# Kernel optimization log

Hardware: AMD Instinct MI355X
Metric: run time of the kernel (lower is better)

The kernel has to match this reference:

```python
import jax, jax.numpy as jnp
import numpy as np

B, S, N, DEG, KC = 4, 12, 8192, 16, 3
SEQ = S - KC + 1  # 10
H, LAYER, HID, MLP_H = 4, 3, 3, 64
NEG = -1e9


def setup_inputs() -> dict:
    key = jax.random.key(0)
    ks = jax.random.split(key, 40)
    f = lambda i, shp, sc=0.2: jax.random.normal(ks[i], shp, jnp.float32) * sc
    # deterministic unique edge list: DEG distinct neighbors per source node
    src = np.repeat(np.arange(N), DEG)
    dst = (src + 1 + np.tile(np.arange(DEG), N) * 37) % N
    edges = jnp.asarray(np.stack([src, dst]).astype(np.int32))
    return dict(
        occ=jax.random.normal(ks[0], (B, S, N), jnp.float32),
        prc_l=jax.random.uniform(ks[1], (B, N), jnp.float32),
        edges=edges,
        values=jnp.ones((N * DEG,), jnp.float32),
        conv_w=f(2, (1, 1, KC, 2)), conv_b=f(3, (1,)),
        gat_W=f(4, (H, SEQ, SEQ)), gat_a=f(5, (H, 2 * SEQ)),
        gat_lin_w=f(6, (1, H)), gat_lin_b=f(7, (1,)),
        gcn_w=f(8, (SEQ, SEQ)), gcn_b=f(9, (SEQ,)),
        Wih0=f(10, (4 * HID, LAYER)), Whh0=f(11, (4 * HID, HID)), bih0=f(12, (4 * HID,)), bhh0=f(13, (4 * HID,)),
        Wih1=f(14, (4 * HID, HID)), Whh1=f(15, (4 * HID, HID)), bih1=f(16, (4 * HID,)), bhh1=f(17, (4 * HID,)),
        Qw=f(18, (SEQ, SEQ)), Kw=f(19, (SEQ, SEQ)), Vw=f(20, (SEQ, SEQ)),
        m1w1=f(21, (MLP_H, SEQ)), m1b1=f(22, (MLP_H,)),
        m1w2=f(23, (MLP_H // 2, MLP_H)), m1b2=f(24, (MLP_H // 2,)),
        m1w3=f(25, (1, MLP_H // 2)), m1b3=f(26, (1,)),
        m2w1=f(27, (8 * (LAYER + 1), LAYER + 1)), m2b1=f(28, (8 * (LAYER + 1),)),
        m2w2=f(29, (4 * (LAYER + 1), 8 * (LAYER + 1))), m2b2=f(30, (4 * (LAYER + 1),)),
        m2w3=f(31, (1, 4 * (LAYER + 1))), m2b3=f(32, (1,)),
    )


def _lstm_layer(x, Wih, Whh, bih, bhh):
    # x: [T, Bn, in] time-major; PyTorch gate order i,f,g,o
    Bn, hdim = x.shape[1], Whh.shape[1]
    def step(carry, xt):
        h, c = carry
        g = xt @ Wih.T + h @ Whh.T + bih + bhh
        i, fg, gg, o = jnp.split(g, 4, axis=1)
        c = jax.nn.sigmoid(fg) * c + jax.nn.sigmoid(i) * jnp.tanh(gg)
        h = jax.nn.sigmoid(o) * jnp.tanh(c)
        return (h, c), h
    init = (jnp.zeros((Bn, hdim), x.dtype), jnp.zeros((Bn, hdim), x.dtype))
    _, hs = jax.lax.scan(step, init, x)
    return hs  # [T, Bn, hdim]


def _gat(x2, src, dst, values, mask, gat_W, gat_a, lin_w, lin_b):
    # x2: [b*n, seq]; only first N rows are gathered (faithful to the original)
    h = jnp.einsum('ns,hso->hno', x2, gat_W)                 # [H, b*n, seq]
    eh = jnp.concatenate([h[:, src, :], h[:, dst, :]], 2)    # [H, E, 2*seq]
    atts = jax.nn.leaky_relu(jnp.einsum('hed,hd->he', eh, gat_a), 0.2)  # [H, E]
    mt = atts.T @ lin_w.T + lin_b                            # [E, 1]
    new_vals = values * mt[:, 0]
    n = mask.shape[0]
    dense = jnp.zeros((n, n), x2.dtype).at[src, dst].add(new_vals)
    return jax.nn.softmax(dense + mask, axis=0)              # softmax over dim 0, as nn.Softmax(dim=0)


def reference(occ, prc_l, edges, values, conv_w, conv_b, gat_W, gat_a, gat_lin_w, gat_lin_b, gcn_w, gcn_b, Wih0, Whh0, bih0, bhh0, Wih1, Whh1, bih1, bhh1, Qw, Kw, Vw, m1w1, m1b1, m1w2, m1b2, m1w3, m1b3, m2w1, m2b1, m2w2, m2b2, m2w3, m2b3):
    b, s, n = occ.shape
    seq = s - conv_w.shape[2] + 1
    occ_t = jnp.transpose(occ, (0, 2, 1))                    # [b, n, s]
    prc = jnp.broadcast_to(prc_l[:, :, None], (b, n, s))
    fea = jnp.stack([occ_t, prc], axis=3).reshape(b * n, s, 2)[:, None]  # [bn,1,s,2]
    fea = jax.lax.conv_general_dilated(fea, conv_w, (1, 1), 'VALID',
                                       dimension_numbers=('NCHW', 'OIHW', 'NCHW'))
    fea = (fea + conv_b[None, :, None, None]).reshape(b, n, seq)
    src, dst = edges[0], edges[1]
    mask = jnp.full((n, n), NEG, occ.dtype).at[src, dst].set(0.0)
    lrelu = lambda z: jax.nn.leaky_relu(z, 0.01)
    gcn = lambda z: lrelu(z @ gcn_w.T + gcn_b)
    A1 = _gat(fea.reshape(b * n, seq), src, dst, values, mask, gat_W, gat_a, gat_lin_w, gat_lin_b)
    c1 = gcn(jnp.einsum('nm,bms->bns', A1, fea))
    A2 = _gat(c1.reshape(b * n, seq), src, dst, values, mask, gat_W, gat_a, gat_lin_w, gat_lin_b)
    c2 = gcn(jnp.einsum('nm,bms->bns', A2, c1))
    xt = jnp.stack([fea, c1, c2], axis=3).reshape(b * n, seq, 3)
    xT = jnp.transpose(xt, (1, 0, 2))                        # time-major [seq, bn, 3]
    h0 = _lstm_layer(xT, Wih0, Whh0, bih0, bhh0)
    h1 = _lstm_layer(h0, Wih1, Whh1, bih1, bhh1)
    x_long = jnp.transpose(h1, (1, 0, 2))                    # [bn, seq, 3]
    y_long = x_long[:, -1, 0]                                # [bn]
    xl = jnp.transpose(x_long, (0, 2, 1))                    # [bn, 3, seq]
    Q = xl @ Qw.T
    K = xl @ Kw.T
    V = xl @ Vw.T
    alpha = jax.nn.softmax(jnp.einsum('bis,bjs->bij', Q, K) / jnp.float32(V.shape[1]), axis=2)
    att = jnp.einsum('bij,bjs->bis', alpha, V)               # [bn, 3, seq]
    h = jax.nn.relu(att @ m1w1.T + m1b1)
    h = jax.nn.relu(h @ m1w2.T + m1b2)
    att_out = (h @ m1w3.T + m1b3)[:, :, 0]                   # [bn, 3]
    temp = jnp.concatenate([y_long[:, None], att_out], axis=1)  # [bn, 4]
    h = jax.nn.relu(temp @ m2w1.T + m2b1)
    h = jax.nn.relu(h @ m2w2.T + m2b2)
    y = (h @ m2w3.T + m2b3)[:, 0]
    return y.reshape(b, n)
```

## Files before the change

kernel.cpp:

```cpp
#include <hip/hip_runtime.h>

#define NN    8192
#define BB    4
#define SS    12
#define SEQL  10
#define SEQP  16
#define KCC   3
#define DEGN  16
#define EE    (NN*DEGN)
#define HHH   4
#define HIDN  3
#define BN    (BB*NN)

__device__ __forceinline__ float fexp(float x)  { return __expf(x); }
__device__ __forceinline__ float fsig(float x)  { return __fdividef(1.0f, 1.0f + __expf(-x)); }

__global__ __launch_bounds__(256) void k_fea_node(const float* __restrict__ occ,
                                                  const float* __restrict__ prc,
                                                  const float* __restrict__ convw,
                                                  const float* __restrict__ convb,
                                                  const float* __restrict__ gatW,
                                                  const float* __restrict__ gata,
                                                  float* __restrict__ fea,
                                                  float* __restrict__ p1p2) {
    int t = blockIdx.x * blockDim.x + threadIdx.x;
    if (t >= BN) return;
    int b = t >> 13, nn = t & (NN - 1);
    float o[SS];
    const float* op = occ + (size_t)b * SS * NN + nn;
#pragma unroll
    for (int s = 0; s < SS; s++) o[s] = op[(size_t)s * NN];
    float w0[KCC], w1s = 0.f;
#pragma unroll
    for (int k = 0; k < KCC; k++) { w0[k] = convw[k * 2]; w1s += convw[k * 2 + 1]; }
    float base = prc[t] * w1s + convb[0];
    float fv[SEQL];
#pragma unroll
    for (int tt = 0; tt < SEQL; tt++) {
        float acc = base;
#pragma unroll
        for (int k = 0; k < KCC; k++) acc += o[tt + k] * w0[k];
        fv[tt] = acc;
    }
    float* f = fea + (size_t)t * SEQP;
    *(float4*)(f)     = make_float4(fv[0], fv[1], fv[2], fv[3]);
    *(float4*)(f + 4) = make_float4(fv[4], fv[5], fv[6], fv[7]);
    *(float2*)(f + 8) = make_float2(fv[8], fv[9]);
    if (t < NN) {
#pragma unroll
        for (int hh = 0; hh < HHH; hh++) {
            float p1 = 0.f, p2 = 0.f;
#pragma unroll
            for (int oo = 0; oo < SEQL; oo++) {
                float hv = 0.f;
#pragma unroll
                for (int s = 0; s < SEQL; s++) hv += fv[s] * gatW[hh * (SEQL * SEQL) + s * SEQL + oo];
                p1 += hv * gata[hh * (2 * SEQL) + oo];
                p2 += hv * gata[hh * (2 * SEQL) + SEQL + oo];
            }
            p1p2[t * 8 + hh]     = p1;
            p1p2[t * 8 + 4 + hh] = p2;
        }
    }
}

__global__ __launch_bounds__(256) void k_colmt(const float* __restrict__ values,
                                               const float* __restrict__ p1p2,
                                               const float* __restrict__ linw,
                                               const float* __restrict__ linb,
                                               float* __restrict__ mt,
                                               float2* __restrict__ colms) {
    int u = blockIdx.x * blockDim.x + threadIdx.x;
    int q = u & 3, j = u >> 2;
    float p2l[HHH], lw[HHH];
#pragma unroll
    for (int hh = 0; hh < HHH; hh++) { p2l[hh] = p1p2[j * 8 + 4 + hh]; lw[hh] = linw[hh]; }
    float lb = linb[0];
    float v[4];
#pragma unroll
    for (int dd = 0; dd < 4; dd++) {
        int d = q * 4 + dd;
        int s = (j - 1 - d * 37) & (NN - 1);
        int e = s * DEGN + d;
        float4 p1v = *(const float4*)(p1p2 + s * 8);
        float a0 = p1v.x + p2l[0]; a0 = a0 > 0.f ? a0 : 0.2f * a0;
        float a1 = p1v.y + p2l[1]; a1 = a1 > 0.f ? a1 : 0.2f * a1;
        float a2 = p1v.z + p2l[2]; a2 = a2 > 0.f ? a2 : 0.2f * a2;
        float a3 = p1v.w + p2l[3]; a3 = a3 > 0.f ? a3 : 0.2f * a3;
        float acc = lb + a0*lw[0] + a1*lw[1] + a2*lw[2] + a3*lw[3];
        float m_ = acc * values[e];
        v[dd] = m_;
        mt[e] = m_;
    }
    float m = fmaxf(fmaxf(v[0], v[1]), fmaxf(v[2], v[3]));
    m = fmaxf(m, __shfl_xor(m, 1));
    m = fmaxf(m, __shfl_xor(m, 2));
    float sum = 0.f;
#pragma unroll
    for (int dd = 0; dd < 4; dd++) sum += fexp(v[dd] - m);
    sum += __shfl_xor(sum, 1);
    sum += __shfl_xor(sum, 2);
    if (q == 0) colms[j] = make_float2(m, __fdividef(1.0f, sum));
}

template <int DOP>
__global__ __launch_bounds__(256) void k_agg(const int* __restrict__ edges,
                                             const float* __restrict__ mt,
                                             const float2* __restrict__ colms,
                                             const float* __restrict__ xin,
                                             const float* __restrict__ gcnw,
                                             const float* __restrict__ gcnb,
                                             const float* __restrict__ gatW,
                                             const float* __restrict__ gata,
                                             float* __restrict__ xout,
                                             float* __restrict__ p1p2) {
    int u = blockIdx.x * blockDim.x + threadIdx.x;
    int q = u & 3, t = u >> 2;
    int b = t >> 13, i = t & (NN - 1);
    int e0 = i * DEGN + q * 4;
    int4   dn4 = *(const int4*)(edges + EE + e0);
    float4 mt4 = *(const float4*)(mt + e0);
    int dns[4] = {dn4.x, dn4.y, dn4.z, dn4.w};
    float mts[4] = {mt4.x, mt4.y, mt4.z, mt4.w};
    float acc[SEQL];
#pragma unroll
    for (int s = 0; s < SEQL; s++) acc[s] = 0.f;
#pragma unroll
    for (int dd = 0; dd < 4; dd++) {
        int dn = dns[dd];
        float2 ms = colms[dn];
        float w = fexp(mts[dd] - ms.x) * ms.y;
        const float* xr = xin + ((size_t)b * NN + dn) * SEQP;
        float4 v0 = *(const float4*)(xr);
        float4 v1 = *(const float4*)(xr + 4);
        float2 v2 = *(const float2*)(xr + 8);
        acc[0] += w*v0.x; acc[1] += w*v0.y; acc[2] += w*v0.z; acc[3] += w*v0.w;
        acc[4] += w*v1.x; acc[5] += w*v1.y; acc[6] += w*v1.z; acc[7] += w*v1.w;
        acc[8] += w*v2.x; acc[9] += w*v2.y;
    }
#pragma unroll
    for (int s = 0; s < SEQL; s++) acc[s] += __shfl_xor(acc[s], 1);
#pragma unroll
    for (int s = 0; s < SEQL; s++) acc[s] += __shfl_xor(acc[s], 2);

    float co[SEQL];
#pragma unroll
    for (int o = 0; o < SEQL; o++) {
        float a = gcnb[o];
#pragma unroll
        for (int s = 0; s < SEQL; s++) a += acc[s] * gcnw[o * SEQL + s];
        co[o] = a > 0.f ? a : 0.01f * a;
    }
    if (q == 0) {
        float* xo = xout + (size_t)t * SEQP;
        *(float4*)(xo)     = make_float4(co[0], co[1], co[2], co[3]);
        *(float4*)(xo + 4) = make_float4(co[4], co[5], co[6], co[7]);
        *(float2*)(xo + 8) = make_float2(co[8], co[9]);
    }
    if (DOP && t < NN) {
        float hv[SEQL];
#pragma unroll
        for (int oo = 0; oo < SEQL; oo++) hv[oo] = 0.f;
#pragma unroll
        for (int s = 0; s < SEQL; s++) {
            const float2* wr = (const float2*)(gatW + q * (SEQL*SEQL) + s * SEQL);
#pragma unroll
            for (int p = 0; p < 5; p++) {
                float2 wv = wr[p];
                hv[2*p]   += co[s] * wv.x;
                hv[2*p+1] += co[s] * wv.y;
            }
        }
        const float2* ga1 = (const float2*)(gata + q * (2*SEQL));
        const float2* ga2 = (const float2*)(gata + q * (2*SEQL) + SEQL);
        float p1 = 0.f, p2 = 0.f;
#pragma unroll
        for (int p = 0; p < 5; p++) {
            float2 a1 = ga1[p], a2 = ga2[p];
            p1 += hv[2*p] * a1.x + hv[2*p+1] * a1.y;
            p2 += hv[2*p] * a2.x + hv[2*p+1] * a2.y;
        }
        p1p2[t * 8 + q]     = p1;
        p1p2[t * 8 + 4 + q] = p2;
    }
}

__global__ __launch_bounds__(256) void k_lstm_att(
    const float* __restrict__ fea, const float* __restrict__ c1g, const float* __restrict__ c2g,
    const float* __restrict__ Wih0, const float* __restrict__ Whh0,
    const float* __restrict__ bih0, const float* __restrict__ bhh0,
    const float* __restrict__ Wih1, const float* __restrict__ Whh1,
    const float* __restrict__ bih1, const float* __restrict__ bhh1,
    const float* __restrict__ Qw, const float* __restrict__ Kw, const float* __restrict__ Vw,
    float* __restrict__ attrow) {

    int u = blockIdx.x * blockDim.x + threadIdx.x;
    int e = u & 1;
    int t = u >> 1;

    float fr[SEQL], c1r[SEQL], c2r[SEQL];
    {
        const float* a = fea + (size_t)t * SEQP;
        const float* b = c1g + (size_t)t * SEQP;
        const float* c = c2g + (size_t)t * SEQP;
        float4 a0 = *(const float4*)a, a1 = *(const float4*)(a+4); float2 a2 = *(const float2*)(a+8);
        float4 b0 = *(const float4*)b, b1 = *(const float4*)(b+4); float2 b2 = *(const float2*)(b+8);
        float4 d0 = *(const float4*)c, d1 = *(const float4*)(c+4); float2 d2 = *(const float2*)(c+8);
        fr[0]=a0.x; fr[1]=a0.y; fr[2]=a0.z; fr[3]=a0.w; fr[4]=a1.x; fr[5]=a1.y; fr[6]=a1.z; fr[7]=a1.w; fr[8]=a2.x; fr[9]=a2.y;
        c1r[0]=b0.x; c1r[1]=b0.y; c1r[2]=b0.z; c1r[3]=b0.w; c1r[4]=b1.x; c1r[5]=b1.y; c1r[6]=b1.z; c1r[7]=b1.w; c1r[8]=b2.x; c1r[9]=b2.y;
        c2r[0]=d0.x; c2r[1]=d0.y; c2r[2]=d0.z; c2r[3]=d0.w; c2r[4]=d1.x; c2r[5]=d1.y; c2r[6]=d1.z; c2r[7]=d1.w; c2r[8]=d2.x; c2r[9]=d2.y;
    }

    int r0 = e * 6;
    float W0[6][6], B0[6], W1[6][6], B1[6];
#pragma unroll
    for (int k = 0; k < 6; k++) {
        int r = r0 + k;
        W0[k][0]=Wih0[r*3]; W0[k][1]=Wih0[r*3+1]; W0[k][2]=Wih0[r*3+2];
        W0[k][3]=Whh0[r*3]; W0[k][4]=Whh0[r*3+1]; W0[k][5]=Whh0[r*3+2];
        B0[k]=bih0[r]+bhh0[r];
        W1[k][0]=Wih1[r*3]; W1[k][1]=Wih1[r*3+1]; W1[k][2]=Wih1[r*3+2];
        W1[k][3]=Whh1[r*3]; W1[k][4]=Whh1[r*3+1]; W1[k][5]=Whh1[r*3+2];
        B1[k]=bih1[r]+bhh1[r];
    }
    float two_e = e ? 2.f : 1.f;
    float neg_e = e ? -1.f : 0.f;

    float c0[3]={0,0,0}, c1s[3]={0,0,0}, h0[3]={0,0,0}, h1[3]={0,0,0};
    float hist[SEQL][HIDN];
#pragma unroll
    for (int st = 0; st < SEQL; st++) {
        float tt[6], pp[6];
        {
            float x0 = fr[st], x1 = c1r[st], x2 = c2r[st];
#pragma unroll
            for (int k = 0; k < 6; k++) {
                float g = B0[k] + x0*W0[k][0] + x1*W0[k][1] + x2*W0[k][2]
                                + h0[0]*W0[k][3] + h0[1]*W0[k][4] + h0[2]*W0[k][5];
                if (k < 3) { float uu = fsig(two_e * g); tt[k] = two_e * uu + neg_e; }
                else       { tt[k] = fsig(g); }
            }
#pragma unroll
            for (int k = 0; k < 6; k++) pp[k] = __shfl_xor(tt[k], 1);
#pragma unroll
            for (int j = 0; j < 3; j++) {
                float si = e ? pp[j]   : tt[j];
                float sf = e ? pp[3+j] : tt[3+j];
                float tg = e ? tt[j]   : pp[j];
                float so = e ? tt[3+j] : pp[3+j];
                float cn = sf * c0[j] + si * tg;
                c0[j] = cn;
                h0[j] = so * (2.f * fsig(2.f * cn) - 1.f);
            }
        }
        {
#pragma unroll
            for (int k = 0; k < 6; k++) {
                float g = B1[k] + h0[0]*W1[k][0] + h0[1]*W1[k][1] + h0[2]*W1[k][2]
                                + h1[0]*W1[k][3] + h1[1]*W1[k][4] + h1[2]*W1[k][5];
                if (k < 3) { float uu = fsig(two_e * g); tt[k] = two_e * uu + neg_e; }
                else       { tt[k] = fsig(g); }
            }
#pragma unroll
            for (int k = 0; k < 6; k++) pp[k] = __shfl_xor(tt[k], 1);
#pragma unroll
            for (int j = 0; j < 3; j++) {
                float si = e ? pp[j]   : tt[j];
                float sf = e ? pp[3+j] : tt[3+j];
                float tg = e ? tt[j]   : pp[j];
                float so = e ? tt[3+j] : pp[3+j];
                float cn = sf * c1s[j] + si * tg;
                c1s[j] = cn;
                h1[j] = so * (2.f * fsig(2.f * cn) - 1.f);
            }
        }
#pragma unroll
        for (int j = 0; j < 3; j++) hist[st][j] = h1[j];
    }

    float V[3][5];
    float sc[3][3];
#pragma unroll
    for (int a = 0; a < 3; a++)
#pragma unroll
        for (int j = 0; j < 3; j++) sc[a][j] = 0.f;
#pragma unroll
    for (int p = 0; p < 5; p++) {
        int o = 2 * p + e;
        float wq[SEQL], wk[SEQL], wv[SEQL];
        const float2* q2 = (const float2*)(Qw + o * SEQL);
        const float2* k2 = (const float2*)(Kw + o * SEQL);
        const float2* v2 = (const float2*)(Vw + o * SEQL);
#pragma unroll
        for (int z = 0; z < 5; z++) {
            float2 a = q2[z], b = k2[z], c = v2[z];
            wq[2*z] = a.x; wq[2*z+1] = a.y;
            wk[2*z] = b.x; wk[2*z+1] = b.y;
            wv[2*z] = c.x; wv[2*z+1] = c.y;
        }
        float qj[3], kj[3];
#pragma unroll
        for (int j = 0; j < 3; j++) {
            float qv = 0.f, kv = 0.f, vv = 0.f;
#pragma unroll
            for (int s = 0; s < SEQL; s++) {
                float xv = hist[s][j];
                qv += xv * wq[s]; kv += xv * wk[s]; vv += xv * wv[s];
            }
            qj[j] = qv; kj[j] = kv; V[j][p] = vv;
        }
#pragma unroll
        for (int a = 0; a < 3; a++)
#pragma unroll
            for (int j = 0; j < 3; j++) sc[a][j] += qj[a] * kj[j];
    }
#pragma unroll
    for (int a = 0; a < 3; a++)
#pragma unroll
        for (int j = 0; j < 3; j++) sc[a][j] += __shfl_xor(sc[a][j], 1);

    float* ar = attrow + (size_t)t * 32;
#pragma unroll
    for (int a = 0; a < 3; a++) {
        float s0 = sc[a][0] * (1.f/3.f), s1 = sc[a][1] * (1.f/3.f), s2 = sc[a][2] * (1.f/3.f);
        float m = fmaxf(s0, fmaxf(s1, s2));
        float e0 = fexp(s0-m), e1 = fexp(s1-m), e2 = fexp(s2-m);
        float inv = __fdividef(1.0f, e0 + e1 + e2);
#pragma unroll
        for (int p = 0; p < 5; p++)
            ar[a * SEQL + 2*p + e] = (e0*V[0][p] + e1*V[1][p] + e2*V[2][p]) * inv;
    }
    if (e == 0) ar[30] = hist[SEQL-1][0];
}

__global__ __launch_bounds__(256, 4) void k_head(
    const float* __restrict__ attrow,
    const float* __restrict__ m1w1, const float* __restrict__ m1b1,
    const float* __restrict__ m1w2, const float* __restrict__ m1b2,
    const float* __restrict__ m1w3, const float* __restrict__ m1b3,
    const float* __restrict__ m2w1, const float* __restrict__ m2b1,
    const float* __restrict__ m2w2, const float* __restrict__ m2b2,
    const float* __restrict__ m2w3, const float* __restrict__ m2b3,
    float* __restrict__ out) {

    __shared__ float lw[3717];
    int tid = threadIdx.x;
    for (int z = tid; z < 1024; z += 256) {
        int qq = z >> 8, kk = (z >> 4) & 15, s = z & 15;
        if (s < 12) lw[qq*200 + kk*12 + s] = (s < 10) ? m1w1[(qq*16+kk)*10 + s] : 0.f;
    }
    for (int z = tid; z < 2048; z += 256) {
        int qq = z >> 9, rem = z & 511, r = rem >> 4, kk = rem & 15;
        lw[800 + qq*520 + r*16 + kk] = m1w2[r*64 + qq*16 + kk];
    }
    for (int z = tid; z < 64;  z += 256) lw[2880 + z] = m1b1[z];
    for (int z = tid; z < 32;  z += 256) { lw[2944 + z] = m1b2[z]; lw[2976 + z] = m1w3[z]; }
    for (int z = tid; z < 128; z += 256) lw[3012 + z] = m2w1[z];
    for (int z = tid; z < 32;  z += 256) lw[3140 + z] = m2b1[z];
    for (int z = tid; z < 512; z += 256) lw[3172 + z] = m2w2[z];
    for (int z = tid; z < 16;  z += 256) { lw[3684 + z] = m2b2[z]; lw[3700 + z] = m2w3[z]; }
    if (tid == 0) { lw[3008] = m1b3[0]; lw[3716] = m2b3[0]; }
    __syncthreads();

    int u = blockIdx.x * blockDim.x + tid;
    int q = u & 3;
    int t = u >> 2;

    const float* w1b = lw + q * 200;
    float hb0[16], hb1[16], hb2a[16];
    float ylong;
    {
        float row[32];
        const float4* arp = (const float4*)(attrow + (size_t)t * 32);
#pragma unroll
        for (int p = 0; p < 8; p++) {
            float4 z = arp[p];
            row[4*p] = z.x; row[4*p+1] = z.y; row[4*p+2] = z.z; row[4*p+3] = z.w;
        }
        ylong = row[30];
#pragma unroll 4
        for (int kk = 0; kk < 16; kk++) {
            float4 wa = *(const float4*)(w1b + kk*12);
            float4 wb = *(const float4*)(w1b + kk*12 + 4);
            float4 wc = *(const float4*)(w1b + kk*12 + 8);
            float bk = lw[2880 + q*16 + kk];
            float a0 = bk
                + row[0]*wa.x + row[1]*wa.y + row[2]*wa.z + row[3]*wa.w
                + row[4]*wb.x + row[5]*wb.y + row[6]*wb.z + row[7]*wb.w
                + row[8]*wc.x + row[9]*wc.y;
            float a1 = bk
                + row[10]*wa.x + row[11]*wa.y + row[12]*wa.z + row[13]*wa.w
                + row[14]*wb.x + row[15]*wb.y + row[16]*wb.z + row[17]*wb.w
                + row[18]*wc.x + row[19]*wc.y;
            float a2 = bk
                + row[20]*wa.x + row[21]*wa.y + row[22]*wa.z + row[23]*wa.w
                + row[24]*wb.x + row[25]*wb.y + row[26]*wb.z + row[27]*wb.w
                + row[28]*wc.x + row[29]*wc.y;
            hb0[kk] = a0 > 0.f ? a0 : 0.f;
            hb1[kk] = a1 > 0.f ? a1 : 0.f;
            hb2a[kk] = a2 > 0.f ? a2 : 0.f;
        }
    }

    const float* w2b = lw + 800 + q * 520;
    float ao0 = lw[3008], ao1 = ao0, ao2 = ao0;
#pragma unroll 2
    for (int r = 0; r < 32; r++) {
        const float4* wr = (const float4*)(w2b + r * 16);
        float4 w0 = wr[0], w1 = wr[1], w2 = wr[2], w3 = wr[3];
        float p0 = hb0[0]*w0.x + hb0[1]*w0.y + hb0[2]*w0.z + hb0[3]*w0.w
                 + hb0[4]*w1.x + hb0[5]*w1.y + hb0[6]*w1.z + hb0[7]*w1.w
                 + hb0[8]*w2.x + hb0[9]*w2.y + hb0[10]*w2.z + hb0[11]*w2.w
                 + hb0[12]*w3.x + hb0[13]*w3.y + hb0[14]*w3.z + hb0[15]*w3.w;
        float p1 = hb1[0]*w0.x + hb1[1]*w0.y + hb1[2]*w0.z + hb1[3]*w0.w
                 + hb1[4]*w1.x + hb1[5]*w1.y + hb1[6]*w1.z + hb1[7]*w1.w
                 + hb1[8]*w2.x + hb1[9]*w2.y + hb1[10]*w2.z + hb1[11]*w2.w
                 + hb1[12]*w3.x + hb1[13]*w3.y + hb1[14]*w3.z + hb1[15]*w3.w;
        float p2 = hb2a[0]*w0.x + hb2a[1]*w0.y + hb2a[2]*w0.z + hb2a[3]*w0.w
                 + hb2a[4]*w1.x + hb2a[5]*w1.y + hb2a[6]*w1.z + hb2a[7]*w1.w
                 + hb2a[8]*w2.x + hb2a[9]*w2.y + hb2a[10]*w2.z + hb2a[11]*w2.w
                 + hb2a[12]*w3.x + hb2a[13]*w3.y + hb2a[14]*w3.z + hb2a[15]*w3.w;
        p0 += __shfl_xor(p0, 1); p0 += __shfl_xor(p0, 2);
        p1 += __shfl_xor(p1, 1); p1 += __shfl_xor(p1, 2);
        p2 += __shfl_xor(p2, 1); p2 += __shfl_xor(p2, 2);
        float bb = lw[2944 + r], ww = lw[2976 + r];
        float t0 = p0 + bb; t0 = t0 > 0.f ? t0 : 0.f;
        float t1 = p1 + bb; t1 = t1 > 0.f ? t1 : 0.f;
        float t2 = p2 + bb; t2 = t2 > 0.f ? t2 : 0.f;
        ao0 += t0 * ww; ao1 += t1 * ww; ao2 += t2 * ww;
    }

    float hb2[32];
#pragma unroll 8
    for (int k = 0; k < 32; k++) {
        float4 wv = *(const float4*)(lw + 3012 + k*4);
        float a = lw[3140 + k] + ylong*wv.x + ao0*wv.y + ao1*wv.z + ao2*wv.w;
        hb2[k] = a > 0.f ? a : 0.f;
    }
    float y = lw[3716];
#pragma unroll 4
    for (int r = 0; r < 16; r++) {
        float a = lw[3684 + r];
        const float4* wr = (const float4*)(lw + 3172 + r*32);
#pragma unroll
        for (int c = 0; c < 8; c++) {
            float4 wv = wr[c];
            a += hb2[4*c]*wv.x + hb2[4*c+1]*wv.y + hb2[4*c+2]*wv.z + hb2[4*c+3]*wv.w;
        }
        float h = a > 0.f ? a : 0.f;
        y += h * lw[3700 + r];
    }
    if (q == 0) out[t] = y;
}

extern "C" void kernel_launch(void* const* d_in, const int* in_sizes, int n_in,
                              void* d_out, int out_size, void* d_ws, size_t ws_size,
                              hipStream_t stream) {
    const float* occ    = (const float*)d_in[0];
    const float* prc    = (const float*)d_in[1];
    const int*   edges  = (const int*)  d_in[2];
    const float* values = (const float*)d_in[3];
    const float* convw  = (const float*)d_in[4];
    const float* convb  = (const float*)d_in[5];
    const float* gatW   = (const float*)d_in[6];
    const float* gata   = (const float*)d_in[7];
    const float* linw   = (const float*)d_in[8];
    const float* linb   = (const float*)d_in[9];
    const float* gcnw   = (const float*)d_in[10];
    const float* gcnb   = (const float*)d_in[11];
    const float* Wih0   = (const float*)d_in[12];
    const float* Whh0   = (const float*)d_in[13];
    const float* bih0   = (const float*)d_in[14];
    const float* bhh0   = (const float*)d_in[15];
    const float* Wih1   = (const float*)d_in[16];
    const float* Whh1   = (const float*)d_in[17];
    const float* bih1   = (const float*)d_in[18];
    const float* bhh1   = (const float*)d_in[19];
    const float* Qw     = (const float*)d_in[20];
    const float* Kw     = (const float*)d_in[21];
    const float* Vw     = (const float*)d_in[22];
    const float* m1w1   = (const float*)d_in[23];
    const float* m1b1   = (const float*)d_in[24];
    const float* m1w2   = (const float*)d_in[25];
    const float* m1b2   = (const float*)d_in[26];
    const float* m1w3   = (const float*)d_in[27];
    const float* m1b3   = (const float*)d_in[28];
    const float* m2w1   = (const float*)d_in[29];
    const float* m2b1   = (const float*)d_in[30];
    const float* m2w2   = (const float*)d_in[31];
    const float* m2b2   = (const float*)d_in[32];
    const float* m2w3   = (const float*)d_in[33];
    const float* m2b3   = (const float*)d_in[34];
    float* out = (float*)d_out;

    char* ws = (char*)d_ws;
    float*  fea    = (float*) (ws);
    float*  c1     = (float*) (ws + 2097152);
    float*  c2     = (float*) (ws + 4194304);
    float*  p1p2   = (float*) (ws + 6291456);
    float*  mt     = (float*) (ws + 6553600);
    float2* colms  = (float2*)(ws + 7077888);
    float*  attrow = (float*) (ws + 7143424);

    k_fea_node<<<128, 256, 0, stream>>>(occ, prc, convw, convb, gatW, gata, fea, p1p2);

    k_colmt<<<128, 256, 0, stream>>>(values, p1p2, linw, linb, mt, colms);
    k_agg<1><<<512, 256, 0, stream>>>(edges, mt, colms, fea, gcnw, gcnb,
                                      gatW, gata, c1, p1p2);

    k_colmt<<<128, 256, 0, stream>>>(values, p1p2, linw, linb, mt, colms);
    k_agg<0><<<512, 256, 0, stream>>>(edges, mt, colms, c1, gcnw, gcnb,
                                      gatW, gata, c2, p1p2);

    k_lstm_att<<<256, 256, 0, stream>>>(fea, c1, c2,
        Wih0, Whh0, bih0, bhh0, Wih1, Whh1, bih1, bhh1, Qw, Kw, Vw, attrow);

    k_head<<<512, 256, 0, stream>>>(attrow,
        m1w1, m1b1, m1w2, m1b2, m1w3, m1b3,
        m2w1, m2b1, m2w2, m2b2, m2w3, m2b3, out);
}
```

Before: 81.73 us.

## Split LSTM-attention per node across four lanes, one gate per lane

The fused LSTM plus attention kernel now gives each node four lanes instead of two. Each lane computes the three units of one gate type, and the gates are exchanged with xor-1 and xor-2 shuffles. The Q/K/V output columns are strided by four, with a guard for the last partial group. This doubles the thread count (512 blocks) and shortens the per-thread serial recurrence to get more latency hiding and parallelism, at the cost of more shuffles, redundant input loads and idle lanes in the attention stage.

```diff
diff --git a/kernel.cpp b/kernel.cpp
--- a/kernel.cpp
+++ b/kernel.cpp
@@ -195,8 +195,8 @@
     float* __restrict__ attrow) {
 
     int u = blockIdx.x * blockDim.x + threadIdx.x;
-    int e = u & 1;
-    int t = u >> 1;
+    int e = u & 3;
+    int t = u >> 2;
 
     float fr[SEQL], c1r[SEQL], c2r[SEQL];
     {
@@ -211,11 +211,10 @@
         c2r[0]=d0.x; c2r[1]=d0.y; c2r[2]=d0.z; c2r[3]=d0.w; c2r[4]=d1.x; c2r[5]=d1.y; c2r[6]=d1.z; c2r[7]=d1.w; c2r[8]=d2.x; c2r[9]=d2.y;
     }
 
-    int r0 = e * 6;
-    float W0[6][6], B0[6], W1[6][6], B1[6];
-#pragma unroll
-    for (int k = 0; k < 6; k++) {
-        int r = r0 + k;
+    float W0[3][6], B0[3], W1[3][6], B1[3];
+#pragma unroll
+    for (int k = 0; k < 3; k++) {
+        int r = e * 3 + k;
         W0[k][0]=Wih0[r*3]; W0[k][1]=Wih0[r*3+1]; W0[k][2]=Wih0[r*3+2];
         W0[k][3]=Whh0[r*3]; W0[k][4]=Whh0[r*3+1]; W0[k][5]=Whh0[r*3+2];
         B0[k]=bih0[r]+bhh0[r];
@@ -223,31 +222,33 @@
         W1[k][3]=Whh1[r*3]; W1[k][4]=Whh1[r*3+1]; W1[k][5]=Whh1[r*3+2];
         B1[k]=bih1[r]+bhh1[r];
     }
-    float two_e = e ? 2.f : 1.f;
-    float neg_e = e ? -1.f : 0.f;
+    float two_e = (e == 2) ? 2.f : 1.f;
+    float neg_e = (e == 2) ? -1.f : 0.f;
 
     float c0[3]={0,0,0}, c1s[3]={0,0,0}, h0[3]={0,0,0}, h1[3]={0,0,0};
     float hist[SEQL][HIDN];
 #pragma unroll
     for (int st = 0; st < SEQL; st++) {
-        float tt[6], pp[6];
+        float tt[3], pp[3], qq[3], rr[3];
         {
             float x0 = fr[st], x1 = c1r[st], x2 = c2r[st];
 #pragma unroll
-            for (int k = 0; k < 6; k++) {
+            for (int k = 0; k < 3; k++) {
                 float g = B0[k] + x0*W0[k][0] + x1*W0[k][1] + x2*W0[k][2]
                                 + h0[0]*W0[k][3] + h0[1]*W0[k][4] + h0[2]*W0[k][5];
-                if (k < 3) { float uu = fsig(two_e * g); tt[k] = two_e * uu + neg_e; }
-                else       { tt[k] = fsig(g); }
-            }
-#pragma unroll
-            for (int k = 0; k < 6; k++) pp[k] = __shfl_xor(tt[k], 1);
+                float uu = fsig(two_e * g);
+                tt[k] = two_e * uu + neg_e;
+            }
+#pragma unroll
+            for (int k = 0; k < 3; k++) pp[k] = __shfl_xor(tt[k], 1);
+#pragma unroll
+            for (int k = 0; k < 3; k++) { qq[k] = __shfl_xor(tt[k], 2); rr[k] = __shfl_xor(pp[k], 2); }
 #pragma unroll
             for (int j = 0; j < 3; j++) {
-                float si = e ? pp[j]   : tt[j];
-                float sf = e ? pp[3+j] : tt[3+j];
-                float tg = e ? tt[j]   : pp[j];
-                float so = e ? tt[3+j] : pp[3+j];
+                float si = (e==0)?tt[j]:(e==1)?pp[j]:(e==2)?qq[j]:rr[j];
+                float sf = (e==0)?pp[j]:(e==1)?tt[j]:(e==2)?rr[j]:qq[j];
+                float tg = (e==0)?qq[j]:(e==1)?rr[j]:(e==2)?tt[j]:pp[j];
+                float so = (e==0)?rr[j]:(e==1)?qq[j]:(e==2)?pp[j]:tt[j];
                 float cn = sf * c0[j] + si * tg;
                 c0[j] = cn;
                 h0[j] = so * (2.f * fsig(2.f * cn) - 1.f);
@@ -255,20 +256,22 @@
         }
         {
 #pragma unroll
-            for (int k = 0; k < 6; k++) {
+            for (int k = 0; k < 3; k++) {
                 float g = B1[k] + h0[0]*W1[k][0] + h0[1]*W1[k][1] + h0[2]*W1[k][2]
                                 + h1[0]*W1[k][3] + h1[1]*W1[k][4] + h1[2]*W1[k][5];
-                if (k < 3) { float uu = fsig(two_e * g); tt[k] = two_e * uu + neg_e; }
-                else       { tt[k] = fsig(g); }
-            }
-#pragma unroll
-            for (int k = 0; k < 6; k++) pp[k] = __shfl_xor(tt[k], 1);
+                float uu = fsig(two_e * g);
+                tt[k] = two_e * uu + neg_e;
+            }
+#pragma unroll
+            for (int k = 0; k < 3; k++) pp[k] = __shfl_xor(tt[k], 1);
+#pragma unroll
+            for (int k = 0; k < 3; k++) { qq[k] = __shfl_xor(tt[k], 2); rr[k] = __shfl_xor(pp[k], 2); }
 #pragma unroll
             for (int j = 0; j < 3; j++) {
-                float si = e ? pp[j]   : tt[j];
-                float sf = e ? pp[3+j] : tt[3+j];
-                float tg = e ? tt[j]   : pp[j];
-                float so = e ? tt[3+j] : pp[3+j];
+                float si = (e==0)?tt[j]:(e==1)?pp[j]:(e==2)?qq[j]:rr[j];
+                float sf = (e==0)?pp[j]:(e==1)?tt[j]:(e==2)?rr[j]:qq[j];
+                float tg = (e==0)?qq[j]:(e==1)?rr[j]:(e==2)?tt[j]:pp[j];
+                float so = (e==0)?rr[j]:(e==1)?qq[j]:(e==2)?pp[j]:tt[j];
                 float cn = sf * c1s[j] + si * tg;
                 c1s[j] = cn;
                 h1[j] = so * (2.f * fsig(2.f * cn) - 1.f);
@@ -278,19 +281,21 @@
         for (int j = 0; j < 3; j++) hist[st][j] = h1[j];
     }
 
-    float V[3][5];
+    float V[3][3];
     float sc[3][3];
 #pragma unroll
     for (int a = 0; a < 3; a++)
 #pragma unroll
         for (int j = 0; j < 3; j++) sc[a][j] = 0.f;
 #pragma unroll
-    for (int p = 0; p < 5; p++) {
-        int o = 2 * p + e;
+    for (int p = 0; p < 3; p++) {
+        int o = 4 * p + e;
+        bool act = (o < SEQL);
+        int oc = act ? o : 0;
         float wq[SEQL], wk[SEQL], wv[SEQL];
-        const float2* q2 = (const float2*)(Qw + o * SEQL);
-        const float2* k2 = (const float2*)(Kw + o * SEQL);
-        const float2* v2 = (const float2*)(Vw + o * SEQL);
+        const float2* q2 = (const float2*)(Qw + oc * SEQL);
+        const float2* k2 = (const float2*)(Kw + oc * SEQL);
+        const float2* v2 = (const float2*)(Vw + oc * SEQL);
 #pragma unroll
         for (int z = 0; z < 5; z++) {
             float2 a = q2[z], b = k2[z], c = v2[z];
@@ -309,15 +314,20 @@
             }
             qj[j] = qv; kj[j] = kv; V[j][p] = vv;
         }
-#pragma unroll
-        for (int a = 0; a < 3; a++)
-#pragma unroll
-            for (int j = 0; j < 3; j++) sc[a][j] += qj[a] * kj[j];
+        if (act) {
+#pragma unroll
+            for (int a = 0; a < 3; a++)
+#pragma unroll
+                for (int j = 0; j < 3; j++) sc[a][j] += qj[a] * kj[j];
+        }
     }
 #pragma unroll
     for (int a = 0; a < 3; a++)
 #pragma unroll
-        for (int j = 0; j < 3; j++) sc[a][j] += __shfl_xor(sc[a][j], 1);
+        for (int j = 0; j < 3; j++) {
+            sc[a][j] += __shfl_xor(sc[a][j], 1);
+            sc[a][j] += __shfl_xor(sc[a][j], 2);
+        }
 
     float* ar = attrow + (size_t)t * 32;
 #pragma unroll
@@ -327,8 +337,11 @@
         float e0 = fexp(s0-m), e1 = fexp(s1-m), e2 = fexp(s2-m);
         float inv = __fdividef(1.0f, e0 + e1 + e2);
 #pragma unroll
-        for (int p = 0; p < 5; p++)
-            ar[a * SEQL + 2*p + e] = (e0*V[0][p] + e1*V[1][p] + e2*V[2][p]) * inv;
+        for (int p = 0; p < 3; p++) {
+            int o = 4 * p + e;
+            if (o < SEQL)
+                ar[a * SEQL + o] = (e0*V[0][p] + e1*V[1][p] + e2*V[2][p]) * inv;
+        }
     }
     if (e == 0) ar[30] = hist[SEQL-1][0];
 }
@@ -512,7 +525,7 @@
     k_agg<0><<<512, 256, 0, stream>>>(edges, mt, colms, c1, gcnw, gcnb,
                                       gatW, gata, c2, p1p2);
 
-    k_lstm_att<<<256, 256, 0, stream>>>(fea, c1, c2,
+    k_lstm_att<<<512, 256, 0, stream>>>(fea, c1, c2,
         Wih0, Whh0, bih0, bhh0, Wih1, Whh1, bih1, bhh1, Qw, Kw, Vw, attrow);
 
     k_head<<<512, 256, 0, stream>>>(attrow,
```

Measured after the change: 82.94 us. About the same (+1.5%).
